# Kernel optimization log

Measured on AMD Instinct MI355X. Metric: run time of the kernel, lower is better.

The kernel has to match this reference:

```python
import jax, jax.numpy as jnp
import numpy as np

N, E, L, F, HID, OUT = 20000, 200000, 5, 4, 128, 3


def _lin(x, w, b):
    # torch Linear convention: w is [out, in]
    return x @ w.T + b


def setup_inputs() -> dict:
    key = jax.random.key(0)
    ks = iter(jax.random.split(key, 40))
    nrm = lambda shape, s=0.05: jax.random.normal(next(ks), shape, dtype=jnp.float32) * s
    inp = {
        'x': jax.random.normal(next(ks), (N, L, F), dtype=jnp.float32),
        'edge_index': jax.random.randint(next(ks), (2, E), 0, N, dtype=jnp.int64),
        'edge_attr': jax.random.normal(next(ks), (E, F), dtype=jnp.float32),
        'batch': jnp.zeros((N,), dtype=jnp.int64),
        'node_type': jax.random.normal(next(ks), (N, 1), dtype=jnp.float32),
        # PastStateEncoder params
        'emb': nrm((L, F), 1.0),
        'conv_w': nrm((HID, 2 * F, 3)),  # Conv1d(8,128,3) OIW
        'conv_b': nrm((HID,)),
        # FusionLayer Linear(129,128)
        'fuse_w': nrm((HID, HID + 1)), 'fuse_b': nrm((HID,)),
        # gnn1 EdgeModel: Linear(2*128+4,128), Linear(128,128)
        'g1e_w1': nrm((HID, 2 * HID + F)), 'g1e_b1': nrm((HID,)),
        'g1e_w2': nrm((HID, HID)), 'g1e_b2': nrm((HID,)),
        # gnn1 NodeModel: Linear(256,128), Linear(128,128)
        'g1n_w1': nrm((HID, 2 * HID)), 'g1n_b1': nrm((HID,)),
        'g1n_w2': nrm((HID, HID)), 'g1n_b2': nrm((HID,)),
        # gnn2 EdgeModel: Linear(2*128+128,128), Linear(128,128)
        'g2e_w1': nrm((HID, 3 * HID)), 'g2e_b1': nrm((HID,)),
        'g2e_w2': nrm((HID, HID)), 'g2e_b2': nrm((HID,)),
        # gnn2 NodeModel
        'g2n_w1': nrm((HID, 2 * HID)), 'g2n_b1': nrm((HID,)),
        'g2n_w2': nrm((HID, HID)), 'g2n_b2': nrm((HID,)),
        # final_mlp: Linear(128,128), BN(128), Linear(128,3)
        'fm_w1': nrm((HID, HID)), 'fm_b1': nrm((HID,)),
        'bn_g': jnp.ones((HID,), dtype=jnp.float32), 'bn_b': jnp.zeros((HID,), dtype=jnp.float32),
        'fm_w2': nrm((OUT, HID)), 'fm_b2': nrm((OUT,)),
    }
    return inp


def _encoder(x, emb, conv_w, conv_b):
    # x: [N, L, F]; append learned positional embedding -> [N, L, 2F]
    n = x.shape[0]
    xe = jnp.concatenate([x, jnp.broadcast_to(emb[None], (n, L, F))], axis=-1)
    xc = xe.transpose(0, 2, 1)  # [N, 2F, L]
    y = jax.lax.conv_general_dilated(
        xc, conv_w, window_strides=(1,), padding=[(1, 1)],
        dimension_numbers=('NCW', 'OIW', 'NCW'))
    y = y + conv_b[None, :, None]
    return y.mean(axis=-1)  # [N, HID]


def _edge_mlp(src, dst, ea, w1, b1, w2, b2):
    h = jax.nn.relu(_lin(jnp.concatenate([src, dst, ea], axis=1), w1, b1))
    return _lin(h, w2, b2)


def _node_mlp(x_row, ea, w1, b1, w2, b2):
    h = jax.nn.relu(_lin(jnp.concatenate([x_row, ea], axis=1), w1, b1))
    return _lin(h, w2, b2)


def reference(x, edge_index, edge_attr, batch, node_type,
              emb, conv_w, conv_b, fuse_w, fuse_b,
              g1e_w1, g1e_b1, g1e_w2, g1e_b2, g1n_w1, g1n_b1, g1n_w2, g1n_b2,
              g2e_w1, g2e_b1, g2e_w2, g2e_b2, g2n_w1, g2n_b1, g2n_w2, g2n_b2,
              fm_w1, fm_b1, bn_g, bn_b, fm_w2, fm_b2):
    row, col = edge_index[0], edge_index[1]
    h = _encoder(x, emb, conv_w, conv_b)                     # [N,128]
    h = _lin(jnp.concatenate([h, node_type], axis=-1), fuse_w, fuse_b)  # [N,128]
    # gnn1 (MetaLayer: edge model then node model; node model here is per-edge)
    ea = _edge_mlp(h[row], h[col], edge_attr, g1e_w1, g1e_b1, g1e_w2, g1e_b2)  # [E,128]
    h = _node_mlp(h[row], ea, g1n_w1, g1n_b1, g1n_w2, g1n_b2)                  # [E,128]
    # gnn2 (h now lives on edges; indices < N <= E remain valid, matching torch)
    ea = _edge_mlp(h[row], h[col], ea, g2e_w1, g2e_b1, g2e_w2, g2e_b2)
    h = _node_mlp(h[row], ea, g2n_w1, g2n_b1, g2n_w2, g2n_b2)
    # final head on edge_attr: Linear -> BatchNorm1d (training stats) -> ReLU -> Linear
    z = _lin(ea, fm_w1, fm_b1)
    mu = z.mean(axis=0)
    var = z.var(axis=0)  # biased, matches torch BN normalization
    z = (z - mu) * jax.lax.rsqrt(var + 1e-5) * bn_g + bn_b
    z = jax.nn.relu(z)
    return _lin(z, fm_w2, fm_b2)  # [E,3]
```

## Files before the change

### kernel.cpp

```cpp
#include <hip/hip_runtime.h>

#define N_NODES 20000
#define N_EDGES 200000
#define HID 128
#define STR 136
#define NBLK 3125

typedef unsigned short u16;
using bf16x8 = __attribute__((ext_vector_type(8))) __bf16;
using f32x4  = __attribute__((ext_vector_type(4))) float;

__device__ __forceinline__ u16 f2bf(float f) {
  union { float f; unsigned u; } v; v.f = f;
  unsigned u = v.u;
  return (u16)((u + 0x7FFFu + ((u >> 16) & 1u)) >> 16);
}
__device__ __forceinline__ float bf2f(unsigned s) {
  union { unsigned u; float f; } v; v.u = s << 16;
  return v.f;
}
__device__ __forceinline__ bf16x8 ld8(const u16* p) { return *(const bf16x8*)p; }

__device__ __forceinline__ void zero_acc(f32x4 acc[4][2]) {
#pragma unroll
  for (int i = 0; i < 4; ++i) {
    acc[i][0] = (f32x4){0.f, 0.f, 0.f, 0.f};
    acc[i][1] = (f32x4){0.f, 0.f, 0.f, 0.f};
  }
}

template <int KSTEPS, typename AF>
__device__ __forceinline__ void wgemm(const u16* __restrict__ PW, AF afrag,
                                      f32x4 acc[4][2], int lane, int wave) {
  const u16* pb = PW + (wave * 2 * 64 + lane) * 8;
  bf16x8 b0[2], b1[2];
  b0[0] = ld8(pb);
  b1[0] = ld8(pb + 512);
#pragma unroll
  for (int ks = 0; ks < KSTEPS; ++ks) {
    const int cur = ks & 1, nxt = cur ^ 1;
    if (ks + 1 < KSTEPS) {
      b0[nxt] = ld8(pb + (ks + 1) * 4096);
      b1[nxt] = ld8(pb + (ks + 1) * 4096 + 512);
    }
#pragma unroll
    for (int mt = 0; mt < 4; ++mt) {
      bf16x8 a = afrag(ks, mt);
      acc[mt][0] = __builtin_amdgcn_mfma_f32_16x16x32_bf16(a, b0[cur], acc[mt][0], 0, 0, 0);
      acc[mt][1] = __builtin_amdgcn_mfma_f32_16x16x32_bf16(a, b1[cur], acc[mt][1], 0, 0, 0);
    }
  }
}

template <bool RELU>
__device__ __forceinline__ void epi_store(u16* buf, const f32x4 acc[4][2],
                                          const float* __restrict__ bias,
                                          int lane, int wave) {
  const int c = lane & 15, q = lane >> 4;
  const float bb0 = bias[wave * 32 + c], bb1 = bias[wave * 32 + 16 + c];
#pragma unroll
  for (int mt = 0; mt < 4; ++mt)
#pragma unroll
    for (int nt = 0; nt < 2; ++nt) {
      const float bb = nt ? bb1 : bb0;
      const int col = wave * 32 + nt * 16 + c;
#pragma unroll
      for (int r = 0; r < 4; ++r) {
        float v = acc[mt][nt][r] + bb;
        if (RELU) v = fmaxf(v, 0.f);
        buf[(mt * 16 + q * 4 + r) * STR + col] = f2bf(v);
      }
    }
}

__device__ __forceinline__ void flush_buf(const u16* buf, u16* __restrict__ gout,
                                          int e0, int tid) {
#pragma unroll
  for (int it = 0; it < 4; ++it) {
    int cid = tid + it * 256, e = cid >> 4, p = cid & 15;
    uint4 v = *(const uint4*)(buf + e * STR + p * 8);
    *(uint4*)(gout + (size_t)(e0 + e) * HID + p * 8) = v;
  }
}

__device__ __forceinline__ void stage_gather(const int* __restrict__ rowI,
                                             const int* __restrict__ colI,
                                             const u16* __restrict__ htab,
                                             u16* B0, u16* B1,
                                             int e0, int lane, int wave) {
  const int r = lane >> 4, p = lane & 15;
#pragma unroll
  for (int it = 0; it < 8; ++it) {
    int j = wave * 32 + it * 4 + r;
    int e = j & 63;
    int id = (j < 64) ? rowI[e0 + e] : colI[e0 + e];
    uint4 v = *(const uint4*)(htab + (size_t)id * HID + p * 8);
    *(uint4*)(((j < 64) ? B0 : B1) + e * STR + p * 8) = v;
  }
}

__global__ __launch_bounds__(128) void k_prep1(
    const float* __restrict__ emb, const float* __restrict__ conv_w,
    const float* __restrict__ conv_b, const float* __restrict__ fuse_w,
    const float* __restrict__ fuse_b,
    const float* __restrict__ fm_w1, const float* __restrict__ g2e_b2,
    const float* __restrict__ fm_b1, const float* __restrict__ w6,
    float* __restrict__ Mt, float* __restrict__ C0, float* __restrict__ Wnt,
    float* __restrict__ b67, float* __restrict__ W67) {
  __shared__ float red[22][129];
  __shared__ float w7s[128];
  const int o = blockIdx.x;
  const int j = threadIdx.x;
  float A[21];
  {
    float b0 = conv_b[j];
#pragma unroll
    for (int p = 0; p < 5; ++p) {
#pragma unroll
      for (int i = 0; i < 8; ++i) {
        float s = 0.f;
#pragma unroll
        for (int k = 0; k < 3; ++k) {
          int t = p + 1 - k;
          if (t >= 0 && t < 5) s += conv_w[(j * 8 + i) * 3 + k];
        }
        s *= 0.2f;
        if (i < 4) A[p * 4 + i] = s;
        else b0 += emb[p * 4 + (i - 4)] * s;
      }
    }
    A[20] = b0;
  }
  float w = fuse_w[o * 129 + j];
  float w7 = fm_w1[o * 128 + j];
  w7s[j] = w7;
#pragma unroll
  for (int qq = 0; qq < 21; ++qq) red[qq][j] = w * A[qq];
  red[21][j] = w7 * g2e_b2[j];
  __syncthreads();
  if (j < 22) {
    float s = 0.f;
    for (int t = 0; t < 128; ++t) s += red[j][t];
    if (j < 20)      Mt[j * 128 + o] = s;
    else if (j == 20) C0[o] = s + fuse_b[o];
    else              b67[o] = s + fm_b1[o];
  }
  if (j == 0) Wnt[o] = fuse_w[o * 129 + 128];
  float s = 0.f;
  for (int t = 0; t < 128; ++t) s += w7s[t] * w6[t * 128 + j];
  W67[o * 128 + j] = s;
}

struct PackArgs {
  const float* src[6];
  u16* dst[6];
  int Kin[6];
  int ksCum[7];
};

__global__ __launch_bounds__(256) void k_prep2(
    PackArgs pa, const float* __restrict__ x, const float* __restrict__ node_type,
    const float* __restrict__ Mt, const float* __restrict__ C0,
    const float* __restrict__ Wnt, u16* __restrict__ h2) {
  if (blockIdx.x < 41) {
    int bk = blockIdx.x;
    int mi = 0;
    while (bk >= pa.ksCum[mi + 1]) ++mi;
    int ks = bk - pa.ksCum[mi];
    const float* W = pa.src[mi];
    u16* D = pa.dst[mi] + ks * 4096;
    int Kin = pa.Kin[mi];
#pragma unroll
    for (int t = 0; t < 16; ++t) {
      int el = t * 256 + (int)threadIdx.x;
      int j = el & 7, ln = (el >> 3) & 63, ntile = el >> 9;
      int k = ks * 32 + ((ln >> 4) << 3) + j;
      int n = ntile * 16 + (ln & 15);
      float v = (k < Kin) ? W[n * Kin + k] : 0.0f;
      D[el] = f2bf(v);
    }
    return;
  }
  __shared__ float xs[16][20], nts[16], mts[20 * 128];
  const int tid = threadIdx.x;
  const int n0 = ((int)blockIdx.x - 41) * 16;
  for (int i = tid; i < 320; i += 256) xs[i / 20][i % 20] = x[n0 * 20 + i];
  if (tid < 16) nts[tid] = node_type[n0 + tid];
  for (int i = tid; i < 2560; i += 256) mts[i] = Mt[i];
  __syncthreads();
  const int nl = tid >> 4;
  const int c0 = (tid & 15) * 8;
  float nt = nts[nl];
  union { u16 s[8]; uint4 u; } o;
#pragma unroll
  for (int i = 0; i < 8; ++i) {
    int ch = c0 + i;
    float acc = C0[ch] + Wnt[ch] * nt;
#pragma unroll
    for (int qq = 0; qq < 20; ++qq) acc += xs[nl][qq] * mts[qq * 128 + ch];
    o.s[i] = f2bf(acc);
  }
  *(uint4*)(h2 + (size_t)(n0 + nl) * HID + c0) = o.u;
}

__global__ __launch_bounds__(256, 4) void k_gnn1(
    const int* __restrict__ eidx, const float* __restrict__ eattr,
    const u16* __restrict__ h2, const u16* __restrict__ pW1, const u16* __restrict__ pW2,
    const u16* __restrict__ pW3, const u16* __restrict__ pW4, const float* __restrict__ b1,
    const float* __restrict__ b2, const float* __restrict__ b3, const float* __restrict__ b4,
    u16* __restrict__ ea1, u16* __restrict__ h3) {
  __shared__ __align__(16) u16 B0[64 * STR], B1[64 * STR];
  const int tid = threadIdx.x, lane = tid & 63, wave = tid >> 6;
  const int e0 = blockIdx.x * 64;
  const int m = lane & 15, q = lane >> 4;
  const int aoff = m * STR + q * 8;
  const int* rowI = eidx;
  const int* colI = eidx + N_EDGES;

  stage_gather(rowI, colI, h2, B0, B1, e0, lane, wave);

  bf16x8 ef[4];
#pragma unroll
  for (int mt = 0; mt < 4; ++mt) {
    union { u16 s[8]; uint4 u; bf16x8 v; } t;
    t.u = make_uint4(0u, 0u, 0u, 0u);
    if (q == 0) {
      float4 a = *(const float4*)(eattr + (size_t)(e0 + mt * 16 + m) * 4);
      t.s[0] = f2bf(a.x); t.s[1] = f2bf(a.y); t.s[2] = f2bf(a.z); t.s[3] = f2bf(a.w);
    }
    ef[mt] = t.v;
  }
  __syncthreads();

  f32x4 acc[4][2];
  zero_acc(acc);
  wgemm<9>(pW1, [&](int ks, int mt) -> bf16x8 {
    if (ks < 4) return ld8(B0 + aoff + mt * 16 * STR + ks * 32);
    if (ks < 8) return ld8(B1 + aoff + mt * 16 * STR + (ks - 4) * 32);
    return ef[mt];
  }, acc, lane, wave);
  __syncthreads();
  epi_store<true>(B1, acc, b1, lane, wave);
  __syncthreads();

  zero_acc(acc);
  wgemm<4>(pW2, [&](int ks, int mt) -> bf16x8 {
    return ld8(B1 + aoff + mt * 16 * STR + ks * 32);
  }, acc, lane, wave);
  epi_store<false>(B0, acc, b2, lane, wave);
  __syncthreads();
  flush_buf(B0, ea1, e0, tid);

  if (e0 < N_NODES) {
#pragma unroll
    for (int it = 0; it < 4; ++it) {
      int e = wave * 16 + it * 4 + q;
      int id = rowI[e0 + e];
      uint4 v = *(const uint4*)(h2 + (size_t)id * HID + m * 8);
      *(uint4*)(B1 + e * STR + m * 8) = v;
    }
    __syncthreads();

    zero_acc(acc);
    wgemm<8>(pW3, [&](int ks, int mt) -> bf16x8 {
      if (ks < 4) return ld8(B1 + aoff + mt * 16 * STR + ks * 32);
      return ld8(B0 + aoff + mt * 16 * STR + (ks - 4) * 32);
    }, acc, lane, wave);
    __syncthreads();
    epi_store<true>(B1, acc, b3, lane, wave);
    __syncthreads();

    zero_acc(acc);
    wgemm<4>(pW4, [&](int ks, int mt) -> bf16x8 {
      return ld8(B1 + aoff + mt * 16 * STR + ks * 32);
    }, acc, lane, wave);
    epi_store<false>(B0, acc, b4, lane, wave);
    __syncthreads();
    flush_buf(B0, h3, e0, tid);
  }
}

__global__ __launch_bounds__(256, 4) void k_gnn2(
    const int* __restrict__ eidx, const u16* __restrict__ h3, u16* ea1z,
    const u16* __restrict__ pW5, const u16* __restrict__ pW67,
    const float* __restrict__ b5, const float* __restrict__ b67,
    float* __restrict__ partials) {
  __shared__ __align__(16) u16 B0[64 * STR], B1[64 * STR];
  const int tid = threadIdx.x, lane = tid & 63, wave = tid >> 6;
  const int e0 = blockIdx.x * 64;
  const int m = lane & 15, q = lane >> 4;
  const int aoff = m * STR + q * 8;
  const int* rowI = eidx;
  const int* colI = eidx + N_EDGES;

  stage_gather(rowI, colI, h3, B0, B1, e0, lane, wave);
  __syncthreads();

  f32x4 acc[4][2];
  zero_acc(acc);
  wgemm<8>(pW5, [&](int ks, int mt) -> bf16x8 {
    if (ks < 4) return ld8(B0 + aoff + mt * 16 * STR + ks * 32);
    return ld8(B1 + aoff + mt * 16 * STR + (ks - 4) * 32);
  }, acc, lane, wave);
  __syncthreads();

#pragma unroll
  for (int it = 0; it < 4; ++it) {
    int cid = tid + it * 256, e = cid >> 4, p = cid & 15;
    uint4 v = *(const uint4*)(ea1z + (size_t)(e0 + e) * HID + p * 8);
    *(uint4*)(B0 + e * STR + p * 8) = v;
  }
  __syncthreads();

  wgemm<4>(pW5 + 8 * 4096, [&](int ks, int mt) -> bf16x8 {
    return ld8(B0 + aoff + mt * 16 * STR + ks * 32);
  }, acc, lane, wave);
  epi_store<true>(B1, acc, b5, lane, wave);
  __syncthreads();

  zero_acc(acc);
  wgemm<4>(pW67, [&](int ks, int mt) -> bf16x8 {
    return ld8(B1 + aoff + mt * 16 * STR + ks * 32);
  }, acc, lane, wave);

  {
    const int c = lane & 15;
    const float bb0 = b67[wave * 32 + c], bb1 = b67[wave * 32 + 16 + c];
    float s0 = 0.f, q0 = 0.f, s1 = 0.f, q1 = 0.f;
#pragma unroll
    for (int mt = 0; mt < 4; ++mt)
#pragma unroll
      for (int r = 0; r < 4; ++r) {
        float v0 = acc[mt][0][r] + bb0;
        float v1 = acc[mt][1][r] + bb1;
        s0 += v0; q0 += v0 * v0;
        s1 += v1; q1 += v1 * v1;
        int row = mt * 16 + q * 4 + r;
        B0[row * STR + wave * 32 + c] = f2bf(v0);
        B0[row * STR + wave * 32 + 16 + c] = f2bf(v1);
      }
    s0 += __shfl_xor(s0, 16); s0 += __shfl_xor(s0, 32);
    q0 += __shfl_xor(q0, 16); q0 += __shfl_xor(q0, 32);
    s1 += __shfl_xor(s1, 16); s1 += __shfl_xor(s1, 32);
    q1 += __shfl_xor(q1, 16); q1 += __shfl_xor(q1, 32);
    if (lane < 16) {
      int base = (int)blockIdx.x * 256;
      partials[base + wave * 32 + lane] = s0;
      partials[base + wave * 32 + 16 + lane] = s1;
      partials[base + 128 + wave * 32 + lane] = q0;
      partials[base + 128 + wave * 32 + 16 + lane] = q1;
    }
  }
  __syncthreads();
  flush_buf(B0, ea1z, e0, tid);
}

__global__ void k_reduce(const float* __restrict__ partials, float* __restrict__ bnacc,
                         int nrows) {
  int t = threadIdx.x;
  float s = 0.f;
  for (int b = blockIdx.x; b < nrows; b += 64) s += partials[b * 256 + t];
  atomicAdd(&bnacc[t], s);
}

__global__ __launch_bounds__(256) void k_head(const u16* __restrict__ z,
                                              const float* __restrict__ bnacc,
                                              const float* __restrict__ bn_g,
                                              const float* __restrict__ bn_b,
                                              const float* __restrict__ w2,
                                              const float* __restrict__ b2,
                                              float* __restrict__ out) {
  __shared__ float sh_s[128], sh_h[128], sh_w0[128], sh_w1[128], sh_w2[128];
  const int tid = threadIdx.x;
  if (tid < 128) {
    const float inv = 1.0f / (float)N_EDGES;
    float mu = bnacc[tid] * inv;
    float var = bnacc[128 + tid] * inv - mu * mu;
    float sc = bn_g[tid] * rsqrtf(var + 1e-5f);
    sh_s[tid] = sc;
    sh_h[tid] = bn_b[tid] - mu * sc;
    sh_w0[tid] = w2[tid];
    sh_w1[tid] = w2[128 + tid];
    sh_w2[tid] = w2[256 + tid];
  }
  __syncthreads();
  const int lane = tid & 63, wave = tid >> 6;
  const int g = lane >> 4;
  const int p = lane & 15;
  const int c0 = p * 8;
  const float bb0 = b2[0], bb1 = b2[1], bb2 = b2[2];
#pragma unroll 4
  for (int it = 0; it < 16; ++it) {
    int e = (int)blockIdx.x * 256 + wave * 64 + it * 4 + g;
    if (e >= N_EDGES) break;
    uint4 v = *(const uint4*)(z + (size_t)e * HID + c0);
    unsigned wv[4] = {v.x, v.y, v.z, v.w};
    float a0 = 0.f, a1 = 0.f, a2 = 0.f;
#pragma unroll
    for (int k = 0; k < 4; ++k) {
      int ch = c0 + k * 2;
      float lo = bf2f(wv[k] & 0xffffu), hi = bf2f(wv[k] >> 16);
      float r0 = fmaxf(fmaf(lo, sh_s[ch], sh_h[ch]), 0.f);
      float r1 = fmaxf(fmaf(hi, sh_s[ch + 1], sh_h[ch + 1]), 0.f);
      a0 += r0 * sh_w0[ch] + r1 * sh_w0[ch + 1];
      a1 += r0 * sh_w1[ch] + r1 * sh_w1[ch + 1];
      a2 += r0 * sh_w2[ch] + r1 * sh_w2[ch + 1];
    }
#pragma unroll
    for (int off = 1; off < 16; off <<= 1) {
      a0 += __shfl_xor(a0, off);
      a1 += __shfl_xor(a1, off);
      a2 += __shfl_xor(a2, off);
    }
    if (p < 3) out[e * 3 + p] = (p == 0) ? a0 + bb0 : (p == 1) ? a1 + bb1 : a2 + bb2;
  }
}

extern "C" void kernel_launch(void* const* d_in, const int* in_sizes, int n_in,
                              void* d_out, int out_size, void* d_ws, size_t ws_size,
                              hipStream_t stream) {
  const float* x         = (const float*)d_in[0];
  const int* eidx        = (const int*)d_in[1];
  const float* eattr     = (const float*)d_in[2];
  const float* node_type = (const float*)d_in[4];
  const float* emb       = (const float*)d_in[5];
  const float* conv_w    = (const float*)d_in[6];
  const float* conv_b    = (const float*)d_in[7];
  const float* fuse_w    = (const float*)d_in[8];
  const float* fuse_b    = (const float*)d_in[9];
  const float* g1e_w1    = (const float*)d_in[10];
  const float* g1e_b1    = (const float*)d_in[11];
  const float* g1e_w2    = (const float*)d_in[12];
  const float* g1e_b2    = (const float*)d_in[13];
  const float* g1n_w1    = (const float*)d_in[14];
  const float* g1n_b1    = (const float*)d_in[15];
  const float* g1n_w2    = (const float*)d_in[16];
  const float* g1n_b2    = (const float*)d_in[17];
  const float* g2e_w1    = (const float*)d_in[18];
  const float* g2e_b1    = (const float*)d_in[19];
  const float* g2e_w2    = (const float*)d_in[20];
  const float* g2e_b2    = (const float*)d_in[21];
  const float* fm_w1     = (const float*)d_in[26];
  const float* fm_b1     = (const float*)d_in[27];
  const float* bn_g      = (const float*)d_in[28];
  const float* bn_b      = (const float*)d_in[29];
  const float* fm_w2     = (const float*)d_in[30];
  const float* fm_b2     = (const float*)d_in[31];
  float* out = (float*)d_out;

  char* ws = (char*)d_ws;
  size_t off = 0;
  auto take = [&](size_t bytes) {
    void* p = ws + off;
    off = (off + bytes + 255) & ~(size_t)255;
    return p;
  };
  u16* h2   = (u16*)take((size_t)N_NODES * HID * 2);
  u16* h3   = (u16*)take((size_t)20032 * HID * 2);
  u16* ea1z = (u16*)take((size_t)N_EDGES * HID * 2);
  float* Mt    = (float*)take(20 * 128 * 4);
  float* C0    = (float*)take(128 * 4);
  float* Wnt   = (float*)take(128 * 4);
  float* bnacc = (float*)take(256 * 4);
  float* b67   = (float*)take(128 * 4);
  float* W67f  = (float*)take(128 * 128 * 4);
  float* partials = (float*)take((size_t)NBLK * 256 * 4);
  u16* pW1  = (u16*)take(9 * 4096 * 2);
  u16* pW2  = (u16*)take(4 * 4096 * 2);
  u16* pW3  = (u16*)take(8 * 4096 * 2);
  u16* pW4  = (u16*)take(4 * 4096 * 2);
  u16* pW5  = (u16*)take(12 * 4096 * 2);
  u16* pW67 = (u16*)take(4 * 4096 * 2);

  hipMemsetAsync(bnacc, 0, 256 * 4, stream);
  k_prep1<<<128, 128, 0, stream>>>(emb, conv_w, conv_b, fuse_w, fuse_b,
                                   fm_w1, g2e_b2, fm_b1, g2e_w2,
                                   Mt, C0, Wnt, b67, W67f);

  PackArgs pa;
  const float* srcs[6] = {g1e_w1, g1e_w2, g1n_w1, g1n_w2, g2e_w1, W67f};
  u16* dsts[6] = {pW1, pW2, pW3, pW4, pW5, pW67};
  int kins[6] = {260, 128, 256, 128, 384, 128};
  int kst[6] = {9, 4, 8, 4, 12, 4};
  int cum = 0;
  for (int i = 0; i < 6; ++i) {
    pa.src[i] = srcs[i]; pa.dst[i] = dsts[i]; pa.Kin[i] = kins[i];
    pa.ksCum[i] = cum; cum += kst[i];
  }
  pa.ksCum[6] = cum;

  k_prep2<<<41 + N_NODES / 16, 256, 0, stream>>>(pa, x, node_type, Mt, C0, Wnt, h2);
  k_gnn1<<<NBLK, 256, 0, stream>>>(eidx, eattr, h2, pW1, pW2, pW3, pW4,
                                   g1e_b1, g1e_b2, g1n_b1, g1n_b2, ea1z, h3);
  k_gnn2<<<NBLK, 256, 0, stream>>>(eidx, h3, ea1z, pW5, pW67,
                                   g2e_b1, b67, partials);
  k_reduce<<<64, 256, 0, stream>>>(partials, bnacc, NBLK);
  k_head<<<(N_EDGES + 255) / 256, 256, 0, stream>>>(ea1z, bnacc, bn_g, bn_b,
                                                    fm_w2, fm_b2, out);
}
```

Before: 253.5 us.

## Retile wave GEMMs to 2x4 MFMA tiles and read ea1 fragments directly from global

```diff
diff --git a/kernel.cpp b/kernel.cpp
--- a/kernel.cpp
+++ b/kernel.cpp
@@ -21,54 +21,55 @@
 }
 __device__ __forceinline__ bf16x8 ld8(const u16* p) { return *(const bf16x8*)p; }
 
-__device__ __forceinline__ void zero_acc(f32x4 acc[4][2]) {
-#pragma unroll
-  for (int i = 0; i < 4; ++i) {
-    acc[i][0] = (f32x4){0.f, 0.f, 0.f, 0.f};
-    acc[i][1] = (f32x4){0.f, 0.f, 0.f, 0.f};
-  }
+__device__ __forceinline__ void zero_acc(f32x4 acc[2][4]) {
+#pragma unroll
+  for (int i = 0; i < 2; ++i)
+#pragma unroll
+    for (int j = 0; j < 4; ++j) acc[i][j] = (f32x4){0.f, 0.f, 0.f, 0.f};
 }
 
 template <int KSTEPS, typename AF>
 __device__ __forceinline__ void wgemm(const u16* __restrict__ PW, AF afrag,
-                                      f32x4 acc[4][2], int lane, int wave) {
-  const u16* pb = PW + (wave * 2 * 64 + lane) * 8;
-  bf16x8 b0[2], b1[2];
-  b0[0] = ld8(pb);
-  b1[0] = ld8(pb + 512);
+                                      f32x4 acc[2][4], int lane, int ntBase) {
+  const u16* pb = PW + (ntBase * 64 + lane) * 8;
+  bf16x8 b[2][4];
+#pragma unroll
+  for (int j = 0; j < 4; ++j) b[0][j] = ld8(pb + j * 512);
 #pragma unroll
   for (int ks = 0; ks < KSTEPS; ++ks) {
     const int cur = ks & 1, nxt = cur ^ 1;
     if (ks + 1 < KSTEPS) {
-      b0[nxt] = ld8(pb + (ks + 1) * 4096);
-      b1[nxt] = ld8(pb + (ks + 1) * 4096 + 512);
-    }
-#pragma unroll
-    for (int mt = 0; mt < 4; ++mt) {
+#pragma unroll
+      for (int j = 0; j < 4; ++j) b[nxt][j] = ld8(pb + (ks + 1) * 4096 + j * 512);
+    }
+#pragma unroll
+    for (int mt = 0; mt < 2; ++mt) {
       bf16x8 a = afrag(ks, mt);
-      acc[mt][0] = __builtin_amdgcn_mfma_f32_16x16x32_bf16(a, b0[cur], acc[mt][0], 0, 0, 0);
-      acc[mt][1] = __builtin_amdgcn_mfma_f32_16x16x32_bf16(a, b1[cur], acc[mt][1], 0, 0, 0);
+#pragma unroll
+      for (int j = 0; j < 4; ++j)
+        acc[mt][j] = __builtin_amdgcn_mfma_f32_16x16x32_bf16(a, b[cur][j], acc[mt][j], 0, 0, 0);
     }
   }
 }
 
 template <bool RELU>
-__device__ __forceinline__ void epi_store(u16* buf, const f32x4 acc[4][2],
+__device__ __forceinline__ void epi_store(u16* buf, const f32x4 acc[2][4],
                                           const float* __restrict__ bias,
-                                          int lane, int wave) {
+                                          int lane, int mtBase, int ntBase) {
   const int c = lane & 15, q = lane >> 4;
-  const float bb0 = bias[wave * 32 + c], bb1 = bias[wave * 32 + 16 + c];
-#pragma unroll
-  for (int mt = 0; mt < 4; ++mt)
-#pragma unroll
-    for (int nt = 0; nt < 2; ++nt) {
-      const float bb = nt ? bb1 : bb0;
-      const int col = wave * 32 + nt * 16 + c;
+  float bb[4];
+#pragma unroll
+  for (int j = 0; j < 4; ++j) bb[j] = bias[(ntBase + j) * 16 + c];
+#pragma unroll
+  for (int mt = 0; mt < 2; ++mt)
+#pragma unroll
+    for (int j = 0; j < 4; ++j) {
+      const int col = (ntBase + j) * 16 + c;
 #pragma unroll
       for (int r = 0; r < 4; ++r) {
-        float v = acc[mt][nt][r] + bb;
+        float v = acc[mt][j][r] + bb[j];
         if (RELU) v = fmaxf(v, 0.f);
-        buf[(mt * 16 + q * 4 + r) * STR + col] = f2bf(v);
+        buf[((mtBase + mt) * 16 + q * 4 + r) * STR + col] = f2bf(v);
       }
     }
 }
@@ -212,42 +213,43 @@
   __shared__ __align__(16) u16 B0[64 * STR], B1[64 * STR];
   const int tid = threadIdx.x, lane = tid & 63, wave = tid >> 6;
   const int e0 = blockIdx.x * 64;
-  const int m = lane & 15, q = lane >> 4;
-  const int aoff = m * STR + q * 8;
+  const int c = lane & 15, q = lane >> 4;
+  const int mtBase = (wave >> 1) * 2, ntBase = (wave & 1) * 4;
+  const int aoff = c * STR + q * 8;
   const int* rowI = eidx;
   const int* colI = eidx + N_EDGES;
 
   stage_gather(rowI, colI, h2, B0, B1, e0, lane, wave);
 
-  bf16x8 ef[4];
-#pragma unroll
-  for (int mt = 0; mt < 4; ++mt) {
+  bf16x8 ef[2];
+#pragma unroll
+  for (int mt = 0; mt < 2; ++mt) {
     union { u16 s[8]; uint4 u; bf16x8 v; } t;
     t.u = make_uint4(0u, 0u, 0u, 0u);
     if (q == 0) {
-      float4 a = *(const float4*)(eattr + (size_t)(e0 + mt * 16 + m) * 4);
+      float4 a = *(const float4*)(eattr + (size_t)(e0 + (mtBase + mt) * 16 + c) * 4);
       t.s[0] = f2bf(a.x); t.s[1] = f2bf(a.y); t.s[2] = f2bf(a.z); t.s[3] = f2bf(a.w);
     }
     ef[mt] = t.v;
   }
   __syncthreads();
 
-  f32x4 acc[4][2];
+  f32x4 acc[2][4];
   zero_acc(acc);
   wgemm<9>(pW1, [&](int ks, int mt) -> bf16x8 {
-    if (ks < 4) return ld8(B0 + aoff + mt * 16 * STR + ks * 32);
-    if (ks < 8) return ld8(B1 + aoff + mt * 16 * STR + (ks - 4) * 32);
+    if (ks < 4) return ld8(B0 + aoff + (mtBase + mt) * 16 * STR + ks * 32);
+    if (ks < 8) return ld8(B1 + aoff + (mtBase + mt) * 16 * STR + (ks - 4) * 32);
     return ef[mt];
-  }, acc, lane, wave);
-  __syncthreads();
-  epi_store<true>(B1, acc, b1, lane, wave);
+  }, acc, lane, ntBase);
+  __syncthreads();
+  epi_store<true>(B1, acc, b1, lane, mtBase, ntBase);
   __syncthreads();
 
   zero_acc(acc);
   wgemm<4>(pW2, [&](int ks, int mt) -> bf16x8 {
-    return ld8(B1 + aoff + mt * 16 * STR + ks * 32);
-  }, acc, lane, wave);
-  epi_store<false>(B0, acc, b2, lane, wave);
+    return ld8(B1 + aoff + (mtBase + mt) * 16 * STR + ks * 32);
+  }, acc, lane, ntBase);
+  epi_store<false>(B0, acc, b2, lane, mtBase, ntBase);
   __syncthreads();
   flush_buf(B0, ea1, e0, tid);
 
@@ -256,25 +258,25 @@
     for (int it = 0; it < 4; ++it) {
       int e = wave * 16 + it * 4 + q;
       int id = rowI[e0 + e];
-      uint4 v = *(const uint4*)(h2 + (size_t)id * HID + m * 8);
-      *(uint4*)(B1 + e * STR + m * 8) = v;
+      uint4 v = *(const uint4*)(h2 + (size_t)id * HID + c * 8);
+      *(uint4*)(B1 + e * STR + c * 8) = v;
     }
     __syncthreads();
 
     zero_acc(acc);
     wgemm<8>(pW3, [&](int ks, int mt) -> bf16x8 {
-      if (ks < 4) return ld8(B1 + aoff + mt * 16 * STR + ks * 32);
-      return ld8(B0 + aoff + mt * 16 * STR + (ks - 4) * 32);
-    }, acc, lane, wave);
+      if (ks < 4) return ld8(B1 + aoff + (mtBase + mt) * 16 * STR + ks * 32);
+      return ld8(B0 + aoff + (mtBase + mt) * 16 * STR + (ks - 4) * 32);
+    }, acc, lane, ntBase);
     __syncthreads();
-    epi_store<true>(B1, acc, b3, lane, wave);
+    epi_store<true>(B1, acc, b3, lane, mtBase, ntBase);
     __syncthreads();
 
     zero_acc(acc);
     wgemm<4>(pW4, [&](int ks, int mt) -> bf16x8 {
-      return ld8(B1 + aoff + mt * 16 * STR + ks * 32);
-    }, acc, lane, wave);
-    epi_store<false>(B0, acc, b4, lane, wave);
+      return ld8(B1 + aoff + (mtBase + mt) * 16 * STR + ks * 32);
+    }, acc, lane, ntBase);
+    epi_store<false>(B0, acc, b4, lane, mtBase, ntBase);
     __syncthreads();
     flush_buf(B0, h3, e0, tid);
   }
@@ -288,67 +290,62 @@
   __shared__ __align__(16) u16 B0[64 * STR], B1[64 * STR];
   const int tid = threadIdx.x, lane = tid & 63, wave = tid >> 6;
   const int e0 = blockIdx.x * 64;
-  const int m = lane & 15, q = lane >> 4;
-  const int aoff = m * STR + q * 8;
+  const int c = lane & 15, q = lane >> 4;
+  const int mtBase = (wave >> 1) * 2, ntBase = (wave & 1) * 4;
+  const int aoff = c * STR + q * 8;
   const int* rowI = eidx;
   const int* colI = eidx + N_EDGES;
 
   stage_gather(rowI, colI, h3, B0, B1, e0, lane, wave);
   __syncthreads();
 
-  f32x4 acc[4][2];
+  f32x4 acc[2][4];
   zero_acc(acc);
-  wgemm<8>(pW5, [&](int ks, int mt) -> bf16x8 {
-    if (ks < 4) return ld8(B0 + aoff + mt * 16 * STR + ks * 32);
-    return ld8(B1 + aoff + mt * 16 * STR + (ks - 4) * 32);
-  }, acc, lane, wave);
-  __syncthreads();
-
-#pragma unroll
-  for (int it = 0; it < 4; ++it) {
-    int cid = tid + it * 256, e = cid >> 4, p = cid & 15;
-    uint4 v = *(const uint4*)(ea1z + (size_t)(e0 + e) * HID + p * 8);
-    *(uint4*)(B0 + e * STR + p * 8) = v;
-  }
-  __syncthreads();
-
-  wgemm<4>(pW5 + 8 * 4096, [&](int ks, int mt) -> bf16x8 {
-    return ld8(B0 + aoff + mt * 16 * STR + ks * 32);
-  }, acc, lane, wave);
-  epi_store<true>(B1, acc, b5, lane, wave);
+  wgemm<12>(pW5, [&](int ks, int mt) -> bf16x8 {
+    if (ks < 4) return ld8(B0 + aoff + (mtBase + mt) * 16 * STR + ks * 32);
+    if (ks < 8) return ld8(B1 + aoff + (mtBase + mt) * 16 * STR + (ks - 4) * 32);
+    return ld8(ea1z + (size_t)(e0 + (mtBase + mt) * 16 + c) * HID + (ks - 8) * 32 + q * 8);
+  }, acc, lane, ntBase);
+  __syncthreads();
+  epi_store<true>(B1, acc, b5, lane, mtBase, ntBase);
   __syncthreads();
 
   zero_acc(acc);
   wgemm<4>(pW67, [&](int ks, int mt) -> bf16x8 {
-    return ld8(B1 + aoff + mt * 16 * STR + ks * 32);
-  }, acc, lane, wave);
+    return ld8(B1 + aoff + (mtBase + mt) * 16 * STR + ks * 32);
+  }, acc, lane, ntBase);
 
   {
-    const int c = lane & 15;
-    const float bb0 = b67[wave * 32 + c], bb1 = b67[wave * 32 + 16 + c];
-    float s0 = 0.f, q0 = 0.f, s1 = 0.f, q1 = 0.f;
-#pragma unroll
-    for (int mt = 0; mt < 4; ++mt)
-#pragma unroll
-      for (int r = 0; r < 4; ++r) {
-        float v0 = acc[mt][0][r] + bb0;
-        float v1 = acc[mt][1][r] + bb1;
-        s0 += v0; q0 += v0 * v0;
-        s1 += v1; q1 += v1 * v1;
-        int row = mt * 16 + q * 4 + r;
-        B0[row * STR + wave * 32 + c] = f2bf(v0);
-        B0[row * STR + wave * 32 + 16 + c] = f2bf(v1);
+    float bb[4], s[4], sq[4];
+#pragma unroll
+    for (int j = 0; j < 4; ++j) {
+      bb[j] = b67[(ntBase + j) * 16 + c];
+      s[j] = 0.f; sq[j] = 0.f;
+    }
+#pragma unroll
+    for (int mt = 0; mt < 2; ++mt)
+#pragma unroll
+      for (int j = 0; j < 4; ++j) {
+        const int col = (ntBase + j) * 16 + c;
+#pragma unroll
+        for (int r = 0; r < 4; ++r) {
+          float v = acc[mt][j][r] + bb[j];
+          s[j] += v; sq[j] += v * v;
+          B0[((mtBase + mt) * 16 + q * 4 + r) * STR + col] = f2bf(v);
+        }
       }
-    s0 += __shfl_xor(s0, 16); s0 += __shfl_xor(s0, 32);
-    q0 += __shfl_xor(q0, 16); q0 += __shfl_xor(q0, 32);
-    s1 += __shfl_xor(s1, 16); s1 += __shfl_xor(s1, 32);
-    q1 += __shfl_xor(q1, 16); q1 += __shfl_xor(q1, 32);
+#pragma unroll
+    for (int j = 0; j < 4; ++j) {
+      s[j] += __shfl_xor(s[j], 16);  s[j] += __shfl_xor(s[j], 32);
+      sq[j] += __shfl_xor(sq[j], 16); sq[j] += __shfl_xor(sq[j], 32);
+    }
     if (lane < 16) {
-      int base = (int)blockIdx.x * 256;
-      partials[base + wave * 32 + lane] = s0;
-      partials[base + wave * 32 + 16 + lane] = s1;
-      partials[base + 128 + wave * 32 + lane] = q0;
-      partials[base + 128 + wave * 32 + 16 + lane] = q1;
+      int base = (int)blockIdx.x * 512 + (wave >> 1) * 256;
+#pragma unroll
+      for (int j = 0; j < 4; ++j) {
+        partials[base + (ntBase + j) * 16 + lane] = s[j];
+        partials[base + 128 + (ntBase + j) * 16 + lane] = sq[j];
+      }
     }
   }
   __syncthreads();
@@ -464,7 +461,7 @@
   float* bnacc = (float*)take(256 * 4);
   float* b67   = (float*)take(128 * 4);
   float* W67f  = (float*)take(128 * 128 * 4);
-  float* partials = (float*)take((size_t)NBLK * 256 * 4);
+  float* partials = (float*)take((size_t)NBLK * 512 * 4);
   u16* pW1  = (u16*)take(9 * 4096 * 2);
   u16* pW2  = (u16*)take(4 * 4096 * 2);
   u16* pW3  = (u16*)take(8 * 4096 * 2);
@@ -494,7 +491,7 @@
                                    g1e_b1, g1e_b2, g1n_b1, g1n_b2, ea1z, h3);
   k_gnn2<<<NBLK, 256, 0, stream>>>(eidx, h3, ea1z, pW5, pW67,
                                    g2e_b1, b67, partials);
-  k_reduce<<<64, 256, 0, stream>>>(partials, bnacc, NBLK);
+  k_reduce<<<64, 256, 0, stream>>>(partials, bnacc, 2 * NBLK);
   k_head<<<(N_EDGES + 255) / 256, 256, 0, stream>>>(ea1z, bnacc, bn_g, bn_b,
                                                     fm_w2, fm_b2, out);
 }
```

Measured after the change: 268.7 us. +6.0%, slower.

## Merge prep kernels and memset into one launch, recomputing weight folds per block

Applied to the files above, without the earlier changes.

```diff
diff --git a/kernel.cpp b/kernel.cpp
--- a/kernel.cpp
+++ b/kernel.cpp
@@ -99,21 +99,94 @@
   }
 }
 
-__global__ __launch_bounds__(128) void k_prep1(
-    const float* __restrict__ emb, const float* __restrict__ conv_w,
-    const float* __restrict__ conv_b, const float* __restrict__ fuse_w,
-    const float* __restrict__ fuse_b,
-    const float* __restrict__ fm_w1, const float* __restrict__ g2e_b2,
-    const float* __restrict__ fm_b1, const float* __restrict__ w6,
-    float* __restrict__ Mt, float* __restrict__ C0, float* __restrict__ Wnt,
-    float* __restrict__ b67, float* __restrict__ W67) {
-  __shared__ float red[22][129];
-  __shared__ float w7s[128];
-  const int o = blockIdx.x;
-  const int j = threadIdx.x;
-  float A[21];
-  {
-    float b0 = conv_b[j];
+struct PrepArgs {
+  const float* src[5];
+  u16* dst[6];
+  int Kin[6];
+  int ksCum[7];
+  const float *w6, *w7;
+  const float *g2e_b2, *fm_b1;
+  const float *emb, *conv_w, *conv_b, *fuse_w, *fuse_b;
+  const float *x, *node_type;
+  float *b67, *bnacc;
+  u16* h2;
+};
+
+__global__ __launch_bounds__(256) void k_prep(PrepArgs pa) {
+  __shared__ float smemf[8192];
+  const int tid = threadIdx.x;
+  const int bid = blockIdx.x;
+
+  if (bid < 41) {
+    int bk = bid, mi = 0;
+    while (bk >= pa.ksCum[mi + 1]) ++mi;
+    int ks = bk - pa.ksCum[mi];
+    u16* D = pa.dst[mi] + ks * 4096;
+    if (mi == 5) {
+      float* w6s = smemf;
+      float* Wsl = smemf + 4096;
+      const int k0 = ks * 32;
+      const int kk = tid & 31, jg = tid >> 5;
+#pragma unroll
+      for (int rep = 0; rep < 16; ++rep) {
+        int j = jg + rep * 8;
+        w6s[j * 32 + kk] = pa.w6[j * 128 + k0 + kk];
+      }
+      __syncthreads();
+#pragma unroll
+      for (int ni = 0; ni < 16; ++ni) {
+        int n = jg * 16 + ni;
+        float s = 0.f;
+        for (int j = 0; j < 128; ++j) s += pa.w7[n * 128 + j] * w6s[j * 32 + kk];
+        Wsl[n * 32 + kk] = s;
+      }
+      __syncthreads();
+#pragma unroll
+      for (int t = 0; t < 16; ++t) {
+        int el = t * 256 + tid;
+        int j = el & 7, ln = (el >> 3) & 63, ntile = el >> 9;
+        int kkl = ((ln >> 4) << 3) + j;
+        int n = ntile * 16 + (ln & 15);
+        D[el] = f2bf(Wsl[n * 32 + kkl]);
+      }
+      if (ks == 0) {
+        if (tid < 128) {
+          float s = 0.f;
+          for (int j = 0; j < 128; ++j) s += pa.w7[tid * 128 + j] * pa.g2e_b2[j];
+          pa.b67[tid] = s + pa.fm_b1[tid];
+        }
+        pa.bnacc[tid] = 0.f;
+      }
+    } else {
+      const float* W = pa.src[mi];
+      int Kin = pa.Kin[mi];
+#pragma unroll
+      for (int t = 0; t < 16; ++t) {
+        int el = t * 256 + tid;
+        int j = el & 7, ln = (el >> 3) & 63, ntile = el >> 9;
+        int k = ks * 32 + ((ln >> 4) << 3) + j;
+        int n = ntile * 16 + (ln & 15);
+        float v = (k < Kin) ? W[n * Kin + k] : 0.0f;
+        D[el] = f2bf(v);
+      }
+    }
+    return;
+  }
+
+  const int lane = tid & 63, wave = tid >> 6;
+  const int n0 = (bid - 41) * 128;
+  const int ncount = (N_NODES - n0 < 128) ? (N_NODES - n0) : 128;
+  float* As  = smemf;
+  float* mts = As + 2688;
+  float* C0s = mts + 2560;
+  float* Wns = C0s + 128;
+  float* xs  = Wns + 128;
+  float* nts = xs + 2560;
+
+  if (tid < 128) {
+    const int j = tid;
+    float A[21];
+    float b0 = pa.conv_b[j];
 #pragma unroll
     for (int p = 0; p < 5; ++p) {
 #pragma unroll
@@ -122,85 +195,57 @@
 #pragma unroll
         for (int k = 0; k < 3; ++k) {
           int t = p + 1 - k;
-          if (t >= 0 && t < 5) s += conv_w[(j * 8 + i) * 3 + k];
+          if (t >= 0 && t < 5) s += pa.conv_w[(j * 8 + i) * 3 + k];
         }
         s *= 0.2f;
         if (i < 4) A[p * 4 + i] = s;
-        else b0 += emb[p * 4 + (i - 4)] * s;
+        else b0 += pa.emb[p * 4 + (i - 4)] * s;
       }
     }
     A[20] = b0;
-  }
-  float w = fuse_w[o * 129 + j];
-  float w7 = fm_w1[o * 128 + j];
-  w7s[j] = w7;
-#pragma unroll
-  for (int qq = 0; qq < 21; ++qq) red[qq][j] = w * A[qq];
-  red[21][j] = w7 * g2e_b2[j];
-  __syncthreads();
-  if (j < 22) {
-    float s = 0.f;
-    for (int t = 0; t < 128; ++t) s += red[j][t];
-    if (j < 20)      Mt[j * 128 + o] = s;
-    else if (j == 20) C0[o] = s + fuse_b[o];
-    else              b67[o] = s + fm_b1[o];
-  }
-  if (j == 0) Wnt[o] = fuse_w[o * 129 + 128];
-  float s = 0.f;
-  for (int t = 0; t < 128; ++t) s += w7s[t] * w6[t * 128 + j];
-  W67[o * 128 + j] = s;
-}
-
-struct PackArgs {
-  const float* src[6];
-  u16* dst[6];
-  int Kin[6];
-  int ksCum[7];
-};
-
-__global__ __launch_bounds__(256) void k_prep2(
-    PackArgs pa, const float* __restrict__ x, const float* __restrict__ node_type,
-    const float* __restrict__ Mt, const float* __restrict__ C0,
-    const float* __restrict__ Wnt, u16* __restrict__ h2) {
-  if (blockIdx.x < 41) {
-    int bk = blockIdx.x;
-    int mi = 0;
-    while (bk >= pa.ksCum[mi + 1]) ++mi;
-    int ks = bk - pa.ksCum[mi];
-    const float* W = pa.src[mi];
-    u16* D = pa.dst[mi] + ks * 4096;
-    int Kin = pa.Kin[mi];
-#pragma unroll
-    for (int t = 0; t < 16; ++t) {
-      int el = t * 256 + (int)threadIdx.x;
-      int j = el & 7, ln = (el >> 3) & 63, ntile = el >> 9;
-      int k = ks * 32 + ((ln >> 4) << 3) + j;
-      int n = ntile * 16 + (ln & 15);
-      float v = (k < Kin) ? W[n * Kin + k] : 0.0f;
-      D[el] = f2bf(v);
-    }
-    return;
-  }
-  __shared__ float xs[16][20], nts[16], mts[20 * 128];
-  const int tid = threadIdx.x;
-  const int n0 = ((int)blockIdx.x - 41) * 16;
-  for (int i = tid; i < 320; i += 256) xs[i / 20][i % 20] = x[n0 * 20 + i];
-  if (tid < 16) nts[tid] = node_type[n0 + tid];
-  for (int i = tid; i < 2560; i += 256) mts[i] = Mt[i];
-  __syncthreads();
-  const int nl = tid >> 4;
-  const int c0 = (tid & 15) * 8;
-  float nt = nts[nl];
-  union { u16 s[8]; uint4 u; } o;
-#pragma unroll
-  for (int i = 0; i < 8; ++i) {
-    int ch = c0 + i;
-    float acc = C0[ch] + Wnt[ch] * nt;
-#pragma unroll
-    for (int qq = 0; qq < 20; ++qq) acc += xs[nl][qq] * mts[qq * 128 + ch];
-    o.s[i] = f2bf(acc);
-  }
-  *(uint4*)(h2 + (size_t)(n0 + nl) * HID + c0) = o.u;
+#pragma unroll
+    for (int qq = 0; qq < 21; ++qq) As[j * 21 + qq] = A[qq];
+    if (j < ncount) nts[j] = pa.node_type[n0 + j];
+  } else {
+    for (int i = tid - 128; i < ncount * 20; i += 128) xs[i] = pa.x[n0 * 20 + i];
+  }
+  __syncthreads();
+
+  for (int oi = 0; oi < 32; ++oi) {
+    const int o = wave * 32 + oi;
+    float fw0 = pa.fuse_w[o * 129 + lane];
+    float fw1 = pa.fuse_w[o * 129 + 64 + lane];
+#pragma unroll
+    for (int qq = 0; qq < 21; ++qq) {
+      float t = fw0 * As[lane * 21 + qq] + fw1 * As[(lane + 64) * 21 + qq];
+      t += __shfl_xor(t, 1);  t += __shfl_xor(t, 2);  t += __shfl_xor(t, 4);
+      t += __shfl_xor(t, 8);  t += __shfl_xor(t, 16); t += __shfl_xor(t, 32);
+      if (lane == 0) {
+        if (qq < 20) mts[qq * 128 + o] = t;
+        else C0s[o] = t + pa.fuse_b[o];
+      }
+    }
+    if (lane == 0) Wns[o] = pa.fuse_w[o * 129 + 128];
+  }
+  __syncthreads();
+
+  for (int base = 0; base < 128; base += 16) {
+    const int nl = base + (tid >> 4);
+    if (nl < ncount) {
+      const int c0 = (tid & 15) * 8;
+      float nt = nts[nl];
+      union { u16 s[8]; uint4 u; } o;
+#pragma unroll
+      for (int i = 0; i < 8; ++i) {
+        int ch = c0 + i;
+        float acc = C0s[ch] + Wns[ch] * nt;
+#pragma unroll
+        for (int qq = 0; qq < 20; ++qq) acc += xs[nl * 20 + qq] * mts[qq * 128 + ch];
+        o.s[i] = f2bf(acc);
+      }
+      *(uint4*)(pa.h2 + (size_t)(n0 + nl) * HID + c0) = o.u;
+    }
+  }
 }
 
 __global__ __launch_bounds__(256, 4) void k_gnn1(
@@ -458,12 +503,8 @@
   u16* h2   = (u16*)take((size_t)N_NODES * HID * 2);
   u16* h3   = (u16*)take((size_t)20032 * HID * 2);
   u16* ea1z = (u16*)take((size_t)N_EDGES * HID * 2);
-  float* Mt    = (float*)take(20 * 128 * 4);
-  float* C0    = (float*)take(128 * 4);
-  float* Wnt   = (float*)take(128 * 4);
   float* bnacc = (float*)take(256 * 4);
   float* b67   = (float*)take(128 * 4);
-  float* W67f  = (float*)take(128 * 128 * 4);
   float* partials = (float*)take((size_t)NBLK * 256 * 4);
   u16* pW1  = (u16*)take(9 * 4096 * 2);
   u16* pW2  = (u16*)take(4 * 4096 * 2);
@@ -472,24 +513,29 @@
   u16* pW5  = (u16*)take(12 * 4096 * 2);
   u16* pW67 = (u16*)take(4 * 4096 * 2);
 
-  hipMemsetAsync(bnacc, 0, 256 * 4, stream);
-  k_prep1<<<128, 128, 0, stream>>>(emb, conv_w, conv_b, fuse_w, fuse_b,
-                                   fm_w1, g2e_b2, fm_b1, g2e_w2,
-                                   Mt, C0, Wnt, b67, W67f);
-
-  PackArgs pa;
-  const float* srcs[6] = {g1e_w1, g1e_w2, g1n_w1, g1n_w2, g2e_w1, W67f};
+  PrepArgs pa;
+  const float* srcs[5] = {g1e_w1, g1e_w2, g1n_w1, g1n_w2, g2e_w1};
   u16* dsts[6] = {pW1, pW2, pW3, pW4, pW5, pW67};
   int kins[6] = {260, 128, 256, 128, 384, 128};
   int kst[6] = {9, 4, 8, 4, 12, 4};
   int cum = 0;
   for (int i = 0; i < 6; ++i) {
-    pa.src[i] = srcs[i]; pa.dst[i] = dsts[i]; pa.Kin[i] = kins[i];
-    pa.ksCum[i] = cum; cum += kst[i];
+    if (i < 5) pa.src[i] = srcs[i];
+    pa.dst[i] = dsts[i];
+    pa.Kin[i] = kins[i];
+    pa.ksCum[i] = cum;
+    cum += kst[i];
   }
   pa.ksCum[6] = cum;
-
-  k_prep2<<<41 + N_NODES / 16, 256, 0, stream>>>(pa, x, node_type, Mt, C0, Wnt, h2);
+  pa.w6 = g2e_w2; pa.w7 = fm_w1;
+  pa.g2e_b2 = g2e_b2; pa.fm_b1 = fm_b1;
+  pa.emb = emb; pa.conv_w = conv_w; pa.conv_b = conv_b;
+  pa.fuse_w = fuse_w; pa.fuse_b = fuse_b;
+  pa.x = x; pa.node_type = node_type;
+  pa.b67 = b67; pa.bnacc = bnacc; pa.h2 = h2;
+
+  const int NENC = (N_NODES + 127) / 128;
+  k_prep<<<41 + NENC, 256, 0, stream>>>(pa);
   k_gnn1<<<NBLK, 256, 0, stream>>>(eidx, eattr, h2, pW1, pW2, pW3, pW4,
                                    g1e_b1, g1e_b2, g1n_b1, g1n_b2, ea1z, h3);
   k_gnn2<<<NBLK, 256, 0, stream>>>(eidx, h3, ea1z, pW5, pW67,
```

Measured after the change: 410.3 us. +61.9%, slower.
